# Kernel tuning notes

Measured on AMD Instinct MI355X. Metric: run time of the kernel, lower is better.

The kernel has to match this reference:

```python
import jax, jax.numpy as jnp
import numpy as np

B, C, H, W = 16, 512, 96, 96
CH = C // 4  # hidden channels of mask head
TEMPERATURE = 1.0


def setup_inputs() -> dict:
    key = jax.random.key(0)
    k1, k2, k3 = jax.random.split(key, 3)
    x = jax.random.normal(k1, (B, C, H, W), dtype=jnp.float32)
    # 1x1 conv weights stored as (out_ch, in_ch); fan-in scaled init
    w1 = jax.random.normal(k2, (CH, C), dtype=jnp.float32) / np.sqrt(C)
    b1 = jnp.zeros((CH,), dtype=jnp.float32)
    w2 = jax.random.normal(k3, (2, CH), dtype=jnp.float32) / np.sqrt(CH)
    b2 = jnp.zeros((2,), dtype=jnp.float32)
    return {"x": x, "w1": w1, "b1": b1, "w2": w2, "b2": b2}


def reference(x, w1, b1, w2, b2):
    # mask head: 1x1 conv -> ReLU -> 1x1 conv
    h = jnp.einsum('bchw,oc->bohw', x, w1) + b1[None, :, None, None]
    h = jax.nn.relu(h)
    logits = jnp.einsum('bchw,oc->bohw', h, w2) + b2[None, :, None, None]  # (B,2,H,W)
    m = jax.nn.softmax(logits / TEMPERATURE, axis=1)
    x0 = x * m[:, 0:1, :, :]
    x1 = x * m[:, 1:2, :, :]
    return (x0, x1, m)
```

## Files before the change

### kernel.cpp

```cpp
#include <hip/hip_runtime.h>


#define BB   16
#define CC   512
#define HH   96
#define WW   96
#define HWP  (HH * WW)
#define CHN  128
#define XSZ  (BB * CC * HWP)

#define KC   32
#define PXT  128

__global__ __launch_bounds__(256) void mask_head_kernel(
    const float* __restrict__ x, const float* __restrict__ w1,
    const float* __restrict__ b1, const float* __restrict__ w2,
    const float* __restrict__ b2, float* __restrict__ mout)
{
    __shared__ __align__(16) float smem[KC * PXT + KC * CHN];
    float* xs  = smem;
    float* ws  = smem + KC * PXT;
    float* red = smem;

    const int t   = threadIdx.x;
    const int p0  = blockIdx.x * PXT;
    const int b   = p0 / HWP;
    const int hw0 = p0 - b * HWP;

    const int px0 = (t & 15) * 8;
    const int og  = t >> 4;
    const int o0  = og * 8;

    float acc[8][8];
    #pragma unroll
    for (int i = 0; i < 8; ++i)
        #pragma unroll
        for (int j = 0; j < 8; ++j) acc[i][j] = 0.0f;

    const int lpx = (t & 31) * 4;
    const int cst = t >> 5;
    const int ow  = t >> 1;
    const int cbw = (t & 1) * 16;

    for (int c0 = 0; c0 < CC; c0 += KC) {
        __syncthreads();
        #pragma unroll
        for (int r = 0; r < 4; ++r) {
            const int c = cst + r * 8;
            const float4 v =
                *(const float4*)&x[(b * CC + c0 + c) * HWP + hw0 + lpx];
            *(float4*)&xs[c * PXT + lpx] = v;
        }
        {
            const float* wrow = &w1[ow * CC + c0 + cbw];
            #pragma unroll
            for (int k = 0; k < 16; k += 4) {
                const float4 wv = *(const float4*)&wrow[k];
                ws[(cbw + k + 0) * CHN + ow] = wv.x;
                ws[(cbw + k + 1) * CHN + ow] = wv.y;
                ws[(cbw + k + 2) * CHN + ow] = wv.z;
                ws[(cbw + k + 3) * CHN + ow] = wv.w;
            }
        }
        __syncthreads();
        #pragma unroll
        for (int c = 0; c < KC; ++c) {
            const float4 xa = *(const float4*)&xs[c * PXT + px0];
            const float4 xb = *(const float4*)&xs[c * PXT + px0 + 4];
            const float4 wa = *(const float4*)&ws[c * CHN + o0];
            const float4 wb = *(const float4*)&ws[c * CHN + o0 + 4];
            const float xv[8] = {xa.x, xa.y, xa.z, xa.w, xb.x, xb.y, xb.z, xb.w};
            const float wv[8] = {wa.x, wa.y, wa.z, wa.w, wb.x, wb.y, wb.z, wb.w};
            #pragma unroll
            for (int i = 0; i < 8; ++i)
                #pragma unroll
                for (int j = 0; j < 8; ++j)
                    acc[i][j] = fmaf(xv[i], wv[j], acc[i][j]);
        }
    }

    const float4 b1a = *(const float4*)&b1[o0];
    const float4 b1b = *(const float4*)&b1[o0 + 4];
    const float4 w0a = *(const float4*)&w2[o0];
    const float4 w0b = *(const float4*)&w2[o0 + 4];
    const float4 w1a = *(const float4*)&w2[CHN + o0];
    const float4 w1b = *(const float4*)&w2[CHN + o0 + 4];
    const float bbv[8] = {b1a.x, b1a.y, b1a.z, b1a.w, b1b.x, b1b.y, b1b.z, b1b.w};
    const float w0v[8] = {w0a.x, w0a.y, w0a.z, w0a.w, w0b.x, w0b.y, w0b.z, w0b.w};
    const float w1v[8] = {w1a.x, w1a.y, w1a.z, w1a.w, w1b.x, w1b.y, w1b.z, w1b.w};

    float l0p[8], l1p[8];
    #pragma unroll
    for (int i = 0; i < 8; ++i) {
        float l0 = 0.0f, l1 = 0.0f;
        #pragma unroll
        for (int j = 0; j < 8; ++j) {
            const float h  = acc[i][j] + bbv[j];
            const float rl = fmaxf(h, 0.0f);
            l0 = fmaf(rl, w0v[j], l0);
            l1 = fmaf(rl, w1v[j], l1);
        }
        l0p[i] = l0;
        l1p[i] = l1;
    }

    __syncthreads();
    #pragma unroll
    for (int i = 0; i < 8; ++i) {
        red[(og * PXT + px0 + i) * 2 + 0] = l0p[i];
        red[(og * PXT + px0 + i) * 2 + 1] = l1p[i];
    }
    __syncthreads();

    if (t < PXT) {
        float l0 = b2[0], l1 = b2[1];
        #pragma unroll
        for (int g = 0; g < 16; ++g) {
            l0 += red[(g * PXT + t) * 2 + 0];
            l1 += red[(g * PXT + t) * 2 + 1];
        }
        const float d  = l1 - l0;
        const float e  = __expf(d);
        const float m0 = 1.0f / (1.0f + e);
        const float m1 = 1.0f - m0;
        mout[(b * 2 + 0) * HWP + hw0 + t] = m0;
        mout[(b * 2 + 1) * HWP + hw0 + t] = m1;
    }
}

__global__ __launch_bounds__(256) void split_kernel(
    const float* __restrict__ x, const float* __restrict__ m,
    float* __restrict__ out0, float* __restrict__ out1)
{
    const unsigned g   = blockIdx.x * 256u + threadIdx.x;
    const unsigned e   = g * 4u;
    const unsigned bcs = CC * HWP;
    const unsigned b   = e / bcs;
    const unsigned r   = e - b * bcs;
    const unsigned hw  = r % HWP;

    const float4 xv = *(const float4*)&x[e];
    const float4 m0 = *(const float4*)&m[(b * 2u + 0u) * HWP + hw];
    const float4 m1 = *(const float4*)&m[(b * 2u + 1u) * HWP + hw];

    float4 a, c;
    a.x = xv.x * m0.x; a.y = xv.y * m0.y; a.z = xv.z * m0.z; a.w = xv.w * m0.w;
    c.x = xv.x * m1.x; c.y = xv.y * m1.y; c.z = xv.z * m1.z; c.w = xv.w * m1.w;

    *(float4*)&out0[e] = a;
    *(float4*)&out1[e] = c;
}

extern "C" void kernel_launch(void* const* d_in, const int* in_sizes, int n_in,
                              void* d_out, int out_size, void* d_ws, size_t ws_size,
                              hipStream_t stream)
{
    const float* x  = (const float*)d_in[0];
    const float* w1 = (const float*)d_in[1];
    const float* b1 = (const float*)d_in[2];
    const float* w2 = (const float*)d_in[3];
    const float* b2 = (const float*)d_in[4];

    float* out  = (float*)d_out;
    float* out0 = out;
    float* out1 = out + (size_t)XSZ;
    float* mo   = out + (size_t)2 * XSZ;

    mask_head_kernel<<<(BB * HWP) / PXT, 256, 0, stream>>>(x, w1, b1, w2, b2, mo);
    split_kernel<<<XSZ / 4 / 256, 256, 0, stream>>>(x, mo, out0, out1);
}
```

Before: 976.5 us.

## Fuse mask-head and split into one kernel with reverse-order channel reuse

The separate split kernel is removed. Each mask-head block now keeps its 128-pixel softmax mask in shared memory and writes x*m0 and x*m1 for all 512 channels of its pixel tile. The channel loop runs in reverse so the most recently loaded x slices are more likely still in cache, and outputs use nontemporal stores. This drops a second launch, a full re-read of x from a cold cache, and the mask reads, at the cost of a longer serial tail per block.

Result: faster. 897.9 us (-8.1%).

```diff
diff --git a/kernel.cpp b/kernel.cpp
--- a/kernel.cpp
+++ b/kernel.cpp
@@ -12,15 +12,19 @@
 #define KC   32
 #define PXT  128
 
-__global__ __launch_bounds__(256) void mask_head_kernel(
+typedef float v4f __attribute__((ext_vector_type(4)));
+
+__global__ __launch_bounds__(256) void fused_split_kernel(
     const float* __restrict__ x, const float* __restrict__ w1,
     const float* __restrict__ b1, const float* __restrict__ w2,
-    const float* __restrict__ b2, float* __restrict__ mout)
+    const float* __restrict__ b2, float* __restrict__ out0,
+    float* __restrict__ out1, float* __restrict__ mout)
 {
     __shared__ __align__(16) float smem[KC * PXT + KC * CHN];
     float* xs  = smem;
     float* ws  = smem + KC * PXT;
     float* red = smem;
+    float* sm  = smem + KC * PXT;
 
     const int t   = threadIdx.x;
     const int p0  = blockIdx.x * PXT;
@@ -125,30 +129,26 @@
         const float m1 = 1.0f - m0;
         mout[(b * 2 + 0) * HWP + hw0 + t] = m0;
         mout[(b * 2 + 1) * HWP + hw0 + t] = m1;
+        sm[t]       = m0;
+        sm[PXT + t] = m1;
     }
-}
+    __syncthreads();
 
-__global__ __launch_bounds__(256) void split_kernel(
-    const float* __restrict__ x, const float* __restrict__ m,
-    float* __restrict__ out0, float* __restrict__ out1)
-{
-    const unsigned g   = blockIdx.x * 256u + threadIdx.x;
-    const unsigned e   = g * 4u;
-    const unsigned bcs = CC * HWP;
-    const unsigned b   = e / bcs;
-    const unsigned r   = e - b * bcs;
-    const unsigned hw  = r % HWP;
+    const int lpx2 = (t & 31) * 4;
+    const int cr   = t >> 5;
+    const v4f m0v = *(const v4f*)&sm[lpx2];
+    const v4f m1v = *(const v4f*)&sm[PXT + lpx2];
+    const int base = (b * CC) * HWP + hw0 + lpx2;
 
-    const float4 xv = *(const float4*)&x[e];
-    const float4 m0 = *(const float4*)&m[(b * 2u + 0u) * HWP + hw];
-    const float4 m1 = *(const float4*)&m[(b * 2u + 1u) * HWP + hw];
-
-    float4 a, c;
-    a.x = xv.x * m0.x; a.y = xv.y * m0.y; a.z = xv.z * m0.z; a.w = xv.w * m0.w;
-    c.x = xv.x * m1.x; c.y = xv.y * m1.y; c.z = xv.z * m1.z; c.w = xv.w * m1.w;
-
-    *(float4*)&out0[e] = a;
-    *(float4*)&out1[e] = c;
+    #pragma unroll 8
+    for (int c0 = CC - 8; c0 >= 0; c0 -= 8) {
+        const int idx = base + (c0 + cr) * HWP;
+        const v4f xv = *(const v4f*)&x[idx];
+        const v4f a0 = xv * m0v;
+        const v4f a1 = xv * m1v;
+        __builtin_nontemporal_store(a0, (v4f*)&out0[idx]);
+        __builtin_nontemporal_store(a1, (v4f*)&out1[idx]);
+    }
 }
 
 extern "C" void kernel_launch(void* const* d_in, const int* in_sizes, int n_in,
@@ -166,6 +166,6 @@
     float* out1 = out + (size_t)XSZ;
     float* mo   = out + (size_t)2 * XSZ;
 
-    mask_head_kernel<<<(BB * HWP) / PXT, 256, 0, stream>>>(x, w1, b1, w2, b2, mo);
-    split_kernel<<<XSZ / 4 / 256, 256, 0, stream>>>(x, mo, out0, out1);
+    fused_split_kernel<<<(BB * HWP) / PXT, 256, 0, stream>>>(
+        x, w1, b1, w2, b2, out0, out1, mo);
 }
```
